# Performance work log

Hardware: AMD Instinct MI355X
Metric: run time of the kernel (lower is better)

## Reference

```python
import jax, jax.numpy as jnp
import numpy as np

FP8_MAX = 448.0  # max finite value of float8_e4m3fn


def quantize_tensorwise(x):
    """Tensorwise fp8 quantization: returns fp8 tensor and inverse scale."""
    amax = jnp.max(jnp.abs(x))
    inv_scale = jnp.maximum(amax, jnp.asarray(1e-12, x.dtype)) / FP8_MAX
    q = (x / inv_scale).astype(jnp.float8_e4m3fn)
    return q, inv_scale


def setup_inputs() -> dict:
    key = jax.random.key(0)
    k1, k2, k3 = jax.random.split(key, 3)
    x = jax.random.normal(k1, (4, 1024, 4096), dtype=jnp.float32)
    weight = jax.random.normal(k2, (4096, 4096), dtype=jnp.float32) * 0.02
    bias = jax.random.normal(k3, (4096,), dtype=jnp.float32)
    return {"x": x, "weight": weight, "bias": bias}


def reference(x, weight, bias):
    out_shape = (*x.shape[:-1], weight.shape[0])
    xm = x.reshape(-1, x.shape[-1])                    # [M, K]
    fp8_x, x_inv_scale = quantize_tensorwise(xm)       # fp8 input + tensorwise scale
    fp8_wt, w_inv_scale = quantize_tensorwise(weight.T)  # weight.t() quantized, [K, N]
    # fp8 GEMM with inline dequant: (fp8_x @ fp8_w.T) * sx * sw + bias
    acc = jnp.matmul(fp8_x.astype(jnp.float32), fp8_wt.astype(jnp.float32))
    out = acc * (x_inv_scale * w_inv_scale) + bias.astype(jnp.float32)
    return out.reshape(out_shape).astype(x.dtype)
```

## Files before the change

### kernel.cpp

```cpp
#include <hip/hip_runtime.h>
#include <hip/hip_bf16.h>
#include <stdint.h>

static constexpr int M = 4096, N = 4096, K = 4096;
static constexpr float FP8_MAX = 448.0f;

using f32x16 = __attribute__((ext_vector_type(16))) float;
using i32x4  = __attribute__((ext_vector_type(4))) int;
using i32x8  = __attribute__((ext_vector_type(8))) int;

static constexpr size_t AQ_OFF   = 0;
static constexpr size_t BQ_OFF   = (size_t)M * K;
static constexpr size_t AMAX_OFF = BQ_OFF + (size_t)N * K;

__global__ void init_amax_kernel(float* amax) {
    amax[0] = 0.0f;
    amax[1] = 0.0f;
}

__global__ __launch_bounds__(256) void amax_kernel(const float* __restrict__ x,
                                                   const float* __restrict__ w,
                                                   float* __restrict__ amax,
                                                   int n4_per_tensor,
                                                   int blocks_per_tensor) {
    const int tensor = blockIdx.x / blocks_per_tensor;
    const int blk    = blockIdx.x % blocks_per_tensor;
    const float4* src = (const float4*)(tensor == 0 ? x : w);

    float m = 0.0f;
    for (int i = blk * blockDim.x + threadIdx.x; i < n4_per_tensor;
         i += blocks_per_tensor * blockDim.x) {
        float4 v = src[i];
        m = fmaxf(m, fmaxf(fmaxf(fabsf(v.x), fabsf(v.y)),
                           fmaxf(fabsf(v.z), fabsf(v.w))));
    }
    #pragma unroll
    for (int off = 32; off >= 1; off >>= 1)
        m = fmaxf(m, __shfl_xor(m, off, 64));

    __shared__ float sm[4];
    const int lane = threadIdx.x & 63, wid = threadIdx.x >> 6;
    if (lane == 0) sm[wid] = m;
    __syncthreads();
    if (threadIdx.x == 0) {
        m = fmaxf(fmaxf(sm[0], sm[1]), fmaxf(sm[2], sm[3]));
        atomicMax((unsigned int*)&amax[tensor], __float_as_uint(m));
    }
}

__global__ __launch_bounds__(256) void quant_kernel(const float* __restrict__ x,
                                                    const float* __restrict__ w,
                                                    unsigned char* __restrict__ aq,
                                                    unsigned char* __restrict__ bq,
                                                    const float* __restrict__ amax,
                                                    int n4_per_tensor) {
    int gid = blockIdx.x * blockDim.x + threadIdx.x;
    const int tensor = (gid >= n4_per_tensor) ? 1 : 0;
    const int i = tensor ? gid - n4_per_tensor : gid;

    const float inv = fmaxf(amax[tensor], 1e-12f) / FP8_MAX;
    const float4* src = (const float4*)(tensor == 0 ? x : w);
    int* dst = (int*)(tensor == 0 ? aq : bq);

    float4 v = src[i];
    float q0 = v.x / inv, q1 = v.y / inv, q2 = v.z / inv, q3 = v.w / inv;
    int packed = __builtin_amdgcn_cvt_pk_fp8_f32(q0, q1, 0, false);
    packed     = __builtin_amdgcn_cvt_pk_fp8_f32(q2, q3, packed, true);
    dst[i] = packed;
}

static constexpr int BM = 256, BN = 256, BK = 64, DEPTH = 4, NT = K / BK;

__device__ __forceinline__ void gld_lds16(const void* g, void* l) {
    __builtin_amdgcn_global_load_lds(
        (const __attribute__((address_space(1))) void*)g,
        (__attribute__((address_space(3))) void*)l, 16, 0, 0);
}

__global__ __launch_bounds__(512, 2) void gemm_kernel(const unsigned char* __restrict__ Aq,
                                                      const unsigned char* __restrict__ Bq,
                                                      const float* __restrict__ amax,
                                                      const float* __restrict__ bias,
                                                      float* __restrict__ out) {
    __shared__ unsigned char lds[DEPTH][2][BM * BK];

    const int tid  = threadIdx.x;
    const int lane = tid & 63;
    const int w    = tid >> 6;
    const int wr   = w >> 2, wc = w & 3;

    const int bid = blockIdx.x;
    const int swz = (bid & 7) * 32 + (bid >> 3);
    const int brow = (swz >> 4) * BM;
    const int bcol = (swz & 15) * BN;

    const float sx = fmaxf(amax[0], 1e-12f) / FP8_MAX;
    const float sw = fmaxf(amax[1], 1e-12f) / FP8_MAX;
    const float scale = sx * sw;

    const int r4    = lane >> 2;
    const int row0  = w * 16 + r4;
    const int chk   = ((lane & 3) ^ ((row0 >> 1) & 3)) * 16;
    const unsigned char* Abase = Aq + (size_t)brow * K;
    const unsigned char* Bbase = Bq + (size_t)bcol * K;

    const int frow = lane & 31;
    const int swzr = (frow >> 1) & 3;
    const int c0   = (lane >> 5) * 2;
    const int off0 = ((c0 ^ swzr) << 4);
    const int off1 = (((c0 + 1) ^ swzr) << 4);

    f32x16 acc[4][2] = {};

#define STAGE(t, d)                                                              \
    do {                                                                         \
        const int _k0 = (t) * BK;                                                \
        gld_lds16(Abase + (size_t)row0 * K + _k0 + chk,         &lds[d][0][w * 1024]);        \
        gld_lds16(Abase + (size_t)(row0 + 128) * K + _k0 + chk, &lds[d][0][8192 + w * 1024]); \
        gld_lds16(Bbase + (size_t)row0 * K + _k0 + chk,         &lds[d][1][w * 1024]);        \
        gld_lds16(Bbase + (size_t)(row0 + 128) * K + _k0 + chk, &lds[d][1][8192 + w * 1024]); \
    } while (0)

    STAGE(0, 0);
    STAGE(1, 1);
    STAGE(2, 2);

    for (int t = 0; t < NT; ++t) {
        asm volatile("s_waitcnt vmcnt(8)" ::: "memory");
        __builtin_amdgcn_s_barrier();

        const int tn = (t + 3 < NT) ? t + 3 : NT - 1;
        STAGE(tn, (t + 3) & 3);

        const int d = t & 3;
        const unsigned char* Ab = &lds[d][0][0];
        const unsigned char* Bb = &lds[d][1][0];

        i32x8 aF[4], bF[2];
        #pragma unroll
        for (int mt = 0; mt < 4; ++mt) {
            const unsigned char* p = Ab + (wr * 128 + mt * 32 + frow) * BK;
            i32x4 lo = *(const i32x4*)(p + off0);
            i32x4 hi = *(const i32x4*)(p + off1);
            aF[mt] = __builtin_shufflevector(lo, hi, 0, 1, 2, 3, 4, 5, 6, 7);
        }
        #pragma unroll
        for (int nt2 = 0; nt2 < 2; ++nt2) {
            const unsigned char* p = Bb + (wc * 64 + nt2 * 32 + frow) * BK;
            i32x4 lo = *(const i32x4*)(p + off0);
            i32x4 hi = *(const i32x4*)(p + off1);
            bF[nt2] = __builtin_shufflevector(lo, hi, 0, 1, 2, 3, 4, 5, 6, 7);
        }

        __builtin_amdgcn_s_setprio(1);
        #pragma unroll
        for (int mt = 0; mt < 4; ++mt)
            #pragma unroll
            for (int nt2 = 0; nt2 < 2; ++nt2)
                acc[mt][nt2] = __builtin_amdgcn_mfma_scale_f32_32x32x64_f8f6f4(
                    aF[mt], bF[nt2], acc[mt][nt2],
                    0, 0, 0, 0x7F, 0, 0x7F);
        __builtin_amdgcn_s_setprio(0);

        asm volatile("s_waitcnt lgkmcnt(0)" ::: "memory");
        __builtin_amdgcn_sched_barrier(0);
    }
#undef STAGE

    #pragma unroll
    for (int mt = 0; mt < 4; ++mt) {
        const int rbase = brow + wr * 128 + mt * 32 + 4 * (lane >> 5);
        #pragma unroll
        for (int nt2 = 0; nt2 < 2; ++nt2) {
            const int col = bcol + wc * 64 + nt2 * 32 + (lane & 31);
            const float b = bias[col];
            #pragma unroll
            for (int reg = 0; reg < 16; ++reg) {
                const int row = rbase + (reg & 3) + 8 * (reg >> 2);
                out[(size_t)row * N + col] = acc[mt][nt2][reg] * scale + b;
            }
        }
    }
}

extern "C" void kernel_launch(void* const* d_in, const int* in_sizes, int n_in,
                              void* d_out, int out_size, void* d_ws, size_t ws_size,
                              hipStream_t stream) {
    const float* x    = (const float*)d_in[0];
    const float* w    = (const float*)d_in[1];
    const float* bias = (const float*)d_in[2];
    float* out = (float*)d_out;

    unsigned char* aq = (unsigned char*)d_ws + AQ_OFF;
    unsigned char* bq = (unsigned char*)d_ws + BQ_OFF;
    float* amax = (float*)((unsigned char*)d_ws + AMAX_OFF);

    const int n4 = (M * K) / 4;

    init_amax_kernel<<<1, 1, 0, stream>>>(amax);

    const int blocks_per_tensor = 512;
    amax_kernel<<<2 * blocks_per_tensor, 256, 0, stream>>>(x, w, amax, n4, blocks_per_tensor);

    const int quant_blocks = (2 * n4) / 256;
    quant_kernel<<<quant_blocks, 256, 0, stream>>>(x, w, aq, bq, amax, n4);

    gemm_kernel<<<256, 512, 0, stream>>>(aq, bq, amax, bias, out);
}
```

Before: 135.8 us.

## Double-buffer LDS fragment registers to overlap LDS reads with MFMA

Restructures the GEMM main loop into a 4x-unrolled software pipeline with two register fragment sets. Each iteration issues the global-to-LDS prefetch and the LDS reads for the next K-tile, then runs the MFMAs on the fragments loaded in the previous iteration. The goal is to hide LDS read latency behind matrix-core work and to have one barrier per tile, placed after the MFMAs. The cost is an extra fragment set (about 48 VGPRs), which raises register pressure under launch_bounds(512,2) and may cause spills or lower occupancy.

```diff
diff --git a/kernel.cpp b/kernel.cpp
--- a/kernel.cpp
+++ b/kernel.cpp
@@ -77,6 +77,11 @@
         (__attribute__((address_space(3))) void*)l, 16, 0, 0);
 }
 
+struct Frags {
+    i32x8 a[4];
+    i32x8 b[2];
+};
+
 __global__ __launch_bounds__(512, 2) void gemm_kernel(const unsigned char* __restrict__ Aq,
                                                       const unsigned char* __restrict__ Bq,
                                                       const float* __restrict__ amax,
@@ -112,59 +117,81 @@
 
     f32x16 acc[4][2] = {};
 
-#define STAGE(t, d)                                                              \
-    do {                                                                         \
-        const int _k0 = (t) * BK;                                                \
-        gld_lds16(Abase + (size_t)row0 * K + _k0 + chk,         &lds[d][0][w * 1024]);        \
-        gld_lds16(Abase + (size_t)(row0 + 128) * K + _k0 + chk, &lds[d][0][8192 + w * 1024]); \
-        gld_lds16(Bbase + (size_t)row0 * K + _k0 + chk,         &lds[d][1][w * 1024]);        \
-        gld_lds16(Bbase + (size_t)(row0 + 128) * K + _k0 + chk, &lds[d][1][8192 + w * 1024]); \
-    } while (0)
+#define STAGE(t, d)                                                                            \
+    do {                                                                                       \
+        const size_t _k0 = (size_t)(t) * BK;                                                   \
+        gld_lds16(Abase + (size_t)row0 * K + _k0 + chk,         &lds[d][0][w * 1024]);         \
+        gld_lds16(Abase + (size_t)(row0 + 128) * K + _k0 + chk, &lds[d][0][8192 + w * 1024]);  \
+        gld_lds16(Bbase + (size_t)row0 * K + _k0 + chk,         &lds[d][1][w * 1024]);         \
+        gld_lds16(Bbase + (size_t)(row0 + 128) * K + _k0 + chk, &lds[d][1][8192 + w * 1024]);  \
+    } while (0)
+
+#define READ_FRAGS(F, rs)                                                      \
+    do {                                                                       \
+        const unsigned char* _Ab = &lds[rs][0][0];                             \
+        const unsigned char* _Bb = &lds[rs][1][0];                             \
+        _Pragma("unroll")                                                      \
+        for (int _mt = 0; _mt < 4; ++_mt) {                                    \
+            const unsigned char* _p = _Ab + (wr * 128 + _mt * 32 + frow) * BK; \
+            i32x4 _lo = *(const i32x4*)(_p + off0);                            \
+            i32x4 _hi = *(const i32x4*)(_p + off1);                            \
+            F.a[_mt] = __builtin_shufflevector(_lo, _hi, 0, 1, 2, 3, 4, 5, 6, 7); \
+        }                                                                      \
+        _Pragma("unroll")                                                      \
+        for (int _nt = 0; _nt < 2; ++_nt) {                                    \
+            const unsigned char* _p = _Bb + (wc * 64 + _nt * 32 + frow) * BK;  \
+            i32x4 _lo = *(const i32x4*)(_p + off0);                            \
+            i32x4 _hi = *(const i32x4*)(_p + off1);                            \
+            F.b[_nt] = __builtin_shufflevector(_lo, _hi, 0, 1, 2, 3, 4, 5, 6, 7); \
+        }                                                                      \
+    } while (0)
+
+#define MFMA_ALL(F)                                                                 \
+    do {                                                                            \
+        __builtin_amdgcn_s_setprio(1);                                              \
+        _Pragma("unroll")                                                           \
+        for (int _mt = 0; _mt < 4; ++_mt)                                           \
+            _Pragma("unroll")                                                       \
+            for (int _nt = 0; _nt < 2; ++_nt)                                       \
+                acc[_mt][_nt] = __builtin_amdgcn_mfma_scale_f32_32x32x64_f8f6f4(    \
+                    F.a[_mt], F.b[_nt], acc[_mt][_nt], 0, 0, 0, 0x7F, 0, 0x7F);     \
+        __builtin_amdgcn_s_setprio(0);                                              \
+    } while (0)
+
+#define ITER(t, CUR, NXT, rs, ss)                                              \
+    do {                                                                       \
+        STAGE(((t) + 3 < NT) ? (t) + 3 : NT - 1, ss);                          \
+        READ_FRAGS(NXT, rs);                                                   \
+        __builtin_amdgcn_sched_barrier(0);                                     \
+        MFMA_ALL(CUR);                                                         \
+        asm volatile("s_waitcnt lgkmcnt(0)" ::: "memory");                     \
+        __builtin_amdgcn_sched_barrier(0);                                     \
+        asm volatile("s_waitcnt vmcnt(4)" ::: "memory");                       \
+        __builtin_amdgcn_s_barrier();                                          \
+    } while (0)
+
+    Frags fP, fQ;
 
     STAGE(0, 0);
     STAGE(1, 1);
     STAGE(2, 2);
-
-    for (int t = 0; t < NT; ++t) {
-        asm volatile("s_waitcnt vmcnt(8)" ::: "memory");
-        __builtin_amdgcn_s_barrier();
-
-        const int tn = (t + 3 < NT) ? t + 3 : NT - 1;
-        STAGE(tn, (t + 3) & 3);
-
-        const int d = t & 3;
-        const unsigned char* Ab = &lds[d][0][0];
-        const unsigned char* Bb = &lds[d][1][0];
-
-        i32x8 aF[4], bF[2];
-        #pragma unroll
-        for (int mt = 0; mt < 4; ++mt) {
-            const unsigned char* p = Ab + (wr * 128 + mt * 32 + frow) * BK;
-            i32x4 lo = *(const i32x4*)(p + off0);
-            i32x4 hi = *(const i32x4*)(p + off1);
-            aF[mt] = __builtin_shufflevector(lo, hi, 0, 1, 2, 3, 4, 5, 6, 7);
-        }
-        #pragma unroll
-        for (int nt2 = 0; nt2 < 2; ++nt2) {
-            const unsigned char* p = Bb + (wc * 64 + nt2 * 32 + frow) * BK;
-            i32x4 lo = *(const i32x4*)(p + off0);
-            i32x4 hi = *(const i32x4*)(p + off1);
-            bF[nt2] = __builtin_shufflevector(lo, hi, 0, 1, 2, 3, 4, 5, 6, 7);
-        }
-
-        __builtin_amdgcn_s_setprio(1);
-        #pragma unroll
-        for (int mt = 0; mt < 4; ++mt)
-            #pragma unroll
-            for (int nt2 = 0; nt2 < 2; ++nt2)
-                acc[mt][nt2] = __builtin_amdgcn_mfma_scale_f32_32x32x64_f8f6f4(
-                    aF[mt], bF[nt2], acc[mt][nt2],
-                    0, 0, 0, 0x7F, 0, 0x7F);
-        __builtin_amdgcn_s_setprio(0);
-
-        asm volatile("s_waitcnt lgkmcnt(0)" ::: "memory");
-        __builtin_amdgcn_sched_barrier(0);
-    }
+    asm volatile("s_waitcnt vmcnt(8)" ::: "memory");
+    __builtin_amdgcn_s_barrier();
+    READ_FRAGS(fP, 0);
+    asm volatile("s_waitcnt lgkmcnt(0)" ::: "memory");
+    __builtin_amdgcn_sched_barrier(0);
+    asm volatile("s_waitcnt vmcnt(4)" ::: "memory");
+    __builtin_amdgcn_s_barrier();
+
+    for (int t = 0; t < NT; t += 4) {
+        ITER(t + 0, fP, fQ, 1, 3);
+        ITER(t + 1, fQ, fP, 2, 0);
+        ITER(t + 2, fP, fQ, 3, 1);
+        ITER(t + 3, fQ, fP, 0, 2);
+    }
+#undef ITER
+#undef MFMA_ALL
+#undef READ_FRAGS
 #undef STAGE
 
     #pragma unroll
```

Measured after the change: 147.0 us. +8.3%, slower.
